# Kernel optimization log

Measured on AMD Instinct MI355X. Metric: run time of the kernel, lower is better.

## Reference

```python
import jax, jax.numpy as jnp
import numpy as np
from math import sqrt

D_MODEL = 1024
NUM_HEADS = 16
MASK_VAL = -100000000.0


def setup_inputs() -> dict:
    key = jax.random.key(0)
    k1, k2, k3, k4, k5 = jax.random.split(key, 5)
    scale = 1.0 / sqrt(D_MODEL)
    return {
        "in_features": jax.random.normal(k1, (2, 2048, D_MODEL), dtype=jnp.float32),
        "q_proj_weight": jax.random.normal(k2, (D_MODEL, D_MODEL), dtype=jnp.float32) * scale,
        "k_proj_weight": jax.random.normal(k3, (D_MODEL, D_MODEL), dtype=jnp.float32) * scale,
        "v_proj_weight": jax.random.normal(k4, (D_MODEL, D_MODEL), dtype=jnp.float32) * scale,
        "o_proj_weight": jax.random.normal(k5, (D_MODEL, D_MODEL), dtype=jnp.float32) * scale,
    }


def _proj_heads(x, w, h):
    # x: [b, s, d_in], w: [h*d, d_in] -> [b, h, s, d]
    d = w.shape[0] // h
    w = w.reshape(h, d, w.shape[1])
    return jnp.einsum('bsi,hdi->bhsd', x, w)


def reference(in_features, q_proj_weight, k_proj_weight, v_proj_weight, o_proj_weight):
    h = NUM_HEADS
    b, s, _ = in_features.shape
    q = _proj_heads(in_features, q_proj_weight, h)  # [b,h,s,dk]
    k = _proj_heads(in_features, k_proj_weight, h)
    v = _proj_heads(in_features, v_proj_weight, h)
    d_k = q.shape[-1]
    # additive causal mask: -1e8 above diagonal
    mask = jnp.triu(jnp.full((s, s), MASK_VAL, dtype=q.dtype), k=1)[None, None]
    scores = jnp.einsum('bhqd,bhkd->bhqk', q, k) / sqrt(d_k) + mask
    attn = jax.nn.softmax(scores, axis=-1)
    out = jnp.einsum('bhqk,bhkd->bhqd', attn, v)          # [b,h,s,dv]
    out = out.transpose(0, 2, 1, 3).reshape(b, s, -1)      # [b,s,h*dv]
    return jnp.einsum('bsv,mv->bsm', out, o_proj_weight)
```

## Files before the change

### kernel.cpp

```cpp
#include <hip/hip_runtime.h>
#include <hip/hip_bf16.h>
#include <stdint.h>
#include <type_traits>

typedef __bf16 bf16;
typedef __bf16 bf16x4 __attribute__((ext_vector_type(4)));
typedef __bf16 bf16x8 __attribute__((ext_vector_type(8)));
typedef float floatx4 __attribute__((ext_vector_type(4)));
typedef unsigned int u32;

#define D_MODEL 1024
#define SEQ 2048
#define NHEADS 16
#define DH 64
#define BATCH 2
#define MROWS (BATCH * SEQ)

#define XELEMS ((size_t)MROWS * D_MODEL)
#define WELEMS ((size_t)D_MODEL * D_MODEL)
#define CVT_ELEMS (XELEMS + 4 * WELEMS)

__device__ __forceinline__ void gload_lds16(const void* g, void* l) {
  __builtin_amdgcn_global_load_lds(
      (const __attribute__((address_space(1))) u32*)g,
      (__attribute__((address_space(3))) u32*)l, 16, 0, 0);
}

__global__ __launch_bounds__(256) void cvt_f32_bf16(
    const float* __restrict__ s0, const float* __restrict__ s1,
    const float* __restrict__ s2, const float* __restrict__ s3,
    const float* __restrict__ s4, bf16* __restrict__ dst) {
  const size_t i = ((size_t)blockIdx.x * 256 + threadIdx.x) * 8;
  const float* src;
  size_t off;
  if (i < XELEMS) {
    src = s0; off = i;
  } else {
    const size_t j = i - XELEMS;
    const int r = (int)(j / WELEMS);
    src = (r == 0) ? s1 : (r == 1) ? s2 : (r == 2) ? s3 : s4;
    off = j - (size_t)r * WELEMS;
  }
  floatx4 f0 = *(const floatx4*)&src[off];
  floatx4 f1 = *(const floatx4*)&src[off + 4];
  bf16x8 o;
#pragma unroll
  for (int j = 0; j < 4; j++) { o[j] = (bf16)f0[j]; o[4 + j] = (bf16)f1[j]; }
  *(bf16x8*)&dst[i] = o;
}


__global__ __launch_bounds__(256) void gemm_qkv(
    const bf16* __restrict__ A, const bf16* __restrict__ Wq,
    const bf16* __restrict__ Wk, const bf16* __restrict__ Wv,
    bf16* __restrict__ Qo, bf16* __restrict__ Ko, bf16* __restrict__ Vto) {
  const int z = blockIdx.z;
  const bf16* W = (z == 0) ? Wq : (z == 1) ? Wk : Wv;

  __shared__ bf16 As[128 * 64];
  __shared__ bf16 Bs[128 * 64];

  const int tid = threadIdx.x;
  const int lane = tid & 63;
  const int w = tid >> 6;
  const int lo16 = lane & 15;
  const int quad = lane >> 4;
  const int wy = w >> 1, wx = w & 1;

  const int m0 = blockIdx.y * 128;
  const int n0 = blockIdx.x * 128;

  const int sl = lane >> 3;
  const int sc = ((lane & 7) ^ sl) * 8;

  const floatx4 fz = {0.f, 0.f, 0.f, 0.f};
  floatx4 acc[4][4];
#pragma unroll
  for (int i = 0; i < 4; i++)
#pragma unroll
    for (int j = 0; j < 4; j++) acc[i][j] = fz;

  auto kloop = [&](auto vt) {
    constexpr bool VT = decltype(vt)::value;
    for (int k0 = 0; k0 < 1024; k0 += 64) {
      __syncthreads();
#pragma unroll
      for (int i = 0; i < 4; i++) {
        const int seg = i * 4 + w;
        const int row = seg * 8 + sl;
        gload_lds16(&A[(size_t)(m0 + row) * 1024 + k0 + sc], &As[seg * 512]);
        gload_lds16(&W[(size_t)(n0 + row) * 1024 + k0 + sc], &Bs[seg * 512]);
      }
      __syncthreads();

#pragma unroll
      for (int kk = 0; kk < 64; kk += 32) {
        bf16x8 af[4], bfr[4];
        const int cc = (kk >> 3) + quad;
#pragma unroll
        for (int t = 0; t < 4; t++) {
          const int ra = wy * 64 + t * 16 + lo16;
          const int rb = wx * 64 + t * 16 + lo16;
          af[t]  = *(const bf16x8*)&As[ra * 64 + ((cc ^ (ra & 7)) << 3)];
          bfr[t] = *(const bf16x8*)&Bs[rb * 64 + ((cc ^ (rb & 7)) << 3)];
        }
#pragma unroll
        for (int mt = 0; mt < 4; mt++)
#pragma unroll
          for (int nt = 0; nt < 4; nt++) {
            if constexpr (VT)
              acc[mt][nt] = __builtin_amdgcn_mfma_f32_16x16x32_bf16(bfr[nt], af[mt], acc[mt][nt], 0, 0, 0);
            else
              acc[mt][nt] = __builtin_amdgcn_mfma_f32_16x16x32_bf16(af[mt], bfr[nt], acc[mt][nt], 0, 0, 0);
          }
      }
    }
  };
  if (z == 2) kloop(std::true_type{}); else kloop(std::false_type{});

  if (z < 2) {
    bf16* C = (z == 0) ? Qo : Ko;
#pragma unroll
    for (int mt = 0; mt < 4; mt++)
#pragma unroll
      for (int nt = 0; nt < 4; nt++)
#pragma unroll
        for (int r = 0; r < 4; r++) {
          const int row = m0 + wy * 64 + mt * 16 + quad * 4 + r;
          const int col = n0 + wx * 64 + nt * 16 + lo16;
          C[(size_t)row * D_MODEL + col] = (bf16)acc[mt][nt][r];
        }
  } else {
#pragma unroll
    for (int mt = 0; mt < 4; mt++)
#pragma unroll
      for (int nt = 0; nt < 4; nt++)
#pragma unroll
        for (int r = 0; r < 4; r++) {
          const int feat = n0 + wx * 64 + nt * 16 + quad * 4 + r;
          const int tok  = m0 + wy * 64 + mt * 16 + lo16;
          const int hh = feat >> 6, dd = feat & 63;
          const int bb = tok >> 11, ss = tok & 2047;
          Vto[(size_t)((bb * NHEADS + hh) * DH + dd) * SEQ + ss] = (bf16)acc[mt][nt][r];
        }
  }
}

__global__ __launch_bounds__(256) void gemm_o(
    const bf16* __restrict__ A, const bf16* __restrict__ W,
    float* __restrict__ C) {
  __shared__ bf16 As[2 * 64 * 64];
  __shared__ bf16 Bs[2 * 128 * 64];

  const int tid = threadIdx.x;
  const int lane = tid & 63;
  const int w = tid >> 6;
  const int lo16 = lane & 15;
  const int quad = lane >> 4;
  const int wy = w >> 1, wx = w & 1;

  const int m0 = blockIdx.y * 64;
  const int n0 = blockIdx.x * 128;

  const int sl = lane >> 3;
  const int sc = ((lane & 7) ^ sl) * 8;

  const floatx4 fz = {0.f, 0.f, 0.f, 0.f};
  floatx4 acc[2][4];
#pragma unroll
  for (int i = 0; i < 2; i++)
#pragma unroll
    for (int j = 0; j < 4; j++) acc[i][j] = fz;

  for (int k0 = 0; k0 < 1024; k0 += 128) {
    __syncthreads();
#pragma unroll
    for (int kh = 0; kh < 2; kh++) {
#pragma unroll
      for (int i = 0; i < 2; i++) {
        const int seg = i * 4 + w;
        const int row = seg * 8 + sl;
        gload_lds16(&A[(size_t)(m0 + row) * 1024 + k0 + kh * 64 + sc],
                    &As[kh * 4096 + seg * 512]);
      }
#pragma unroll
      for (int i = 0; i < 4; i++) {
        const int seg = i * 4 + w;
        const int row = seg * 8 + sl;
        gload_lds16(&W[(size_t)(n0 + row) * 1024 + k0 + kh * 64 + sc],
                    &Bs[kh * 8192 + seg * 512]);
      }
    }
    __syncthreads();

#pragma unroll
    for (int kk = 0; kk < 128; kk += 32) {
      const int kh = kk >> 6;
      const int cc = ((kk & 63) >> 3) + quad;
      bf16x8 af[2], bfr[4];
#pragma unroll
      for (int t = 0; t < 2; t++) {
        const int ra = wy * 32 + t * 16 + lo16;
        af[t] = *(const bf16x8*)&As[kh * 4096 + ra * 64 + ((cc ^ (ra & 7)) << 3)];
      }
#pragma unroll
      for (int t = 0; t < 4; t++) {
        const int rb = wx * 64 + t * 16 + lo16;
        bfr[t] = *(const bf16x8*)&Bs[kh * 8192 + rb * 64 + ((cc ^ (rb & 7)) << 3)];
      }
#pragma unroll
      for (int mt = 0; mt < 2; mt++)
#pragma unroll
        for (int nt = 0; nt < 4; nt++)
          acc[mt][nt] = __builtin_amdgcn_mfma_f32_16x16x32_bf16(af[mt], bfr[nt], acc[mt][nt], 0, 0, 0);
    }
  }

#pragma unroll
  for (int mt = 0; mt < 2; mt++)
#pragma unroll
    for (int nt = 0; nt < 4; nt++)
#pragma unroll
      for (int r = 0; r < 4; r++) {
        const int row = m0 + wy * 32 + mt * 16 + quad * 4 + r;
        const int col = n0 + wx * 64 + nt * 16 + lo16;
        C[(size_t)row * D_MODEL + col] = acc[mt][nt][r];
      }
}

#define LP 72

__global__ __launch_bounds__(512) void attn_causal(
    const bf16* __restrict__ Q, const bf16* __restrict__ Kg,
    const bf16* __restrict__ Vt, bf16* __restrict__ O) {
  __shared__ bf16 Ks[64 * LP];
  __shared__ bf16 VTs[64 * LP];
  __shared__ bf16 Ps[8][16 * LP];
  __shared__ float Es[4][64][40];

  const int tid = threadIdx.x;
  const int lane = tid & 63;
  const int wid = tid >> 6;
  const int g = wid >> 2;
  const int w4 = wid & 3;
  const int lo16 = lane & 15;
  const int quad = lane >> 4;

  const int x = blockIdx.x;
  const int qtA = x;
  const int qtB = 31 - x;
  const int tmax = qtB;
  const int h = blockIdx.y;
  const int b = blockIdx.z;
  const size_t base  = (size_t)b * SEQ * D_MODEL + (size_t)h * DH;
  const size_t baset = (size_t)(b * NHEADS + h) * DH * SEQ;

  const int rA = qtA * 64 + w4 * 16 + lo16;
  const int rB = qtB * 64 + w4 * 16 + lo16;
  bf16x8 qfA[2], qfB[2];
#pragma unroll
  for (int ks = 0; ks < 2; ks++) {
    qfA[ks] = *(const bf16x8*)&Q[base + (size_t)rA * D_MODEL + ks * 32 + quad * 8];
    qfB[ks] = *(const bf16x8*)&Q[base + (size_t)rB * D_MODEL + ks * 32 + quad * 8];
  }

  bf16x8 onesf;
#pragma unroll
  for (int j = 0; j < 8; j++) onesf[j] = (bf16)1.0f;

  const floatx4 fz = {0.f, 0.f, 0.f, 0.f};
  floatx4 oA[4], oB[4];
  floatx4 lA = fz, lB = fz;
#pragma unroll
  for (int i = 0; i < 4; i++) { oA[i] = fz; oB[i] = fz; }

  const int kr = tid >> 3;
  const int kc = (tid & 7) * 8;

  bf16x8 kv, vv;
  kv = *(const bf16x8*)&Kg[base + (size_t)kr * D_MODEL + kc];
  vv = *(const bf16x8*)&Vt[baset + (size_t)kr * SEQ + kc];

  for (int t = 0; t <= tmax; t++) {
    const int j0 = t * 64;
    __syncthreads();
    *(bf16x8*)&Ks[kr * LP + kc] = kv;
    *(bf16x8*)&VTs[kr * LP + kc] = vv;
    __syncthreads();

    if (t < tmax) {
      const int j1 = j0 + 64;
      kv = *(const bf16x8*)&Kg[base + (size_t)(j1 + kr) * D_MODEL + kc];
      vv = *(const bf16x8*)&Vt[baset + (size_t)kr * SEQ + j1 + kc];
    }

    bf16x8 kf[2][2], vf[4];
#pragma unroll
    for (int n = 0; n < 2; n++)
#pragma unroll
      for (int ks = 0; ks < 2; ks++)
        kf[n][ks] = *(const bf16x8*)&Ks[((2 * g + n) * 16 + lo16) * LP + ks * 32 + quad * 8];
#pragma unroll
    for (int dt = 0; dt < 4; dt++)
      vf[dt] = *(const bf16x8*)&VTs[(dt * 16 + lo16) * LP + g * 32 + quad * 8];

    auto compute = [&](int q0s, const bf16x8* qf, floatx4* oacc, floatx4& lacc,
                       bool diag) {
      floatx4 sacc[2];
#pragma unroll
      for (int n = 0; n < 2; n++) sacc[n] = fz;
#pragma unroll
      for (int n = 0; n < 2; n++)
#pragma unroll
        for (int ks = 0; ks < 2; ks++)
          sacc[n] = __builtin_amdgcn_mfma_f32_16x16x32_bf16(kf[n][ks], qf[ks], sacc[n], 0, 0, 0);

      if (diag) {
        const int myq = q0s + w4 * 16 + lo16;
#pragma unroll
        for (int n = 0; n < 2; n++) {
          const int kvb = j0 + (2 * g + n) * 16 + quad * 4;
          bf16x4 pk;
#pragma unroll
          for (int r = 0; r < 4; r++) {
            const float e = __builtin_amdgcn_exp2f(fmaf(sacc[n][r], 0.18033688f, -17.3123405f));
            pk[r] = (bf16)((kvb + r > myq) ? 0.f : e);
          }
          *(bf16x4*)&Ps[wid][lo16 * LP + n * 16 + quad * 4] = pk;
        }
      } else {
#pragma unroll
        for (int n = 0; n < 2; n++) {
          bf16x4 pk;
#pragma unroll
          for (int r = 0; r < 4; r++)
            pk[r] = (bf16)__builtin_amdgcn_exp2f(fmaf(sacc[n][r], 0.18033688f, -17.3123405f));
          *(bf16x4*)&Ps[wid][lo16 * LP + n * 16 + quad * 4] = pk;
        }
      }

      bf16x8 pf = *(const bf16x8*)&Ps[wid][lo16 * LP + quad * 8];
#pragma unroll
      for (int dt = 0; dt < 4; dt++)
        oacc[dt] = __builtin_amdgcn_mfma_f32_16x16x32_bf16(pf, vf[dt], oacc[dt], 0, 0, 0);
      lacc = __builtin_amdgcn_mfma_f32_16x16x32_bf16(pf, onesf, lacc, 0, 0, 0);
    };

    compute(qtB * 64, qfB, oB, lB, t == qtB);
    if (t <= qtA) compute(qtA * 64, qfA, oA, lA, t == qtA);
  }

  if (g == 1) {
    float* e = Es[w4][lane];
#pragma unroll
    for (int dt = 0; dt < 4; dt++)
#pragma unroll
      for (int r = 0; r < 4; r++) e[dt * 4 + r] = oA[dt][r];
#pragma unroll
    for (int r = 0; r < 4; r++) e[16 + r] = lA[r];
#pragma unroll
    for (int dt = 0; dt < 4; dt++)
#pragma unroll
      for (int r = 0; r < 4; r++) e[20 + dt * 4 + r] = oB[dt][r];
#pragma unroll
    for (int r = 0; r < 4; r++) e[36 + r] = lB[r];
  }
  __syncthreads();
  if (g == 0) {
    const float* e = Es[w4][lane];
#pragma unroll
    for (int dt = 0; dt < 4; dt++)
#pragma unroll
      for (int r = 0; r < 4; r++) { oA[dt][r] += e[dt * 4 + r]; oB[dt][r] += e[20 + dt * 4 + r]; }
#pragma unroll
    for (int r = 0; r < 4; r++) { lA[r] += e[16 + r]; lB[r] += e[36 + r]; }

    auto finish = [&](int q0s, floatx4* oacc, floatx4 lacc) {
#pragma unroll
      for (int r = 0; r < 4; r++) {
        const float inv = 1.0f / lacc[r];
        const int row = q0s + w4 * 16 + quad * 4 + r;
#pragma unroll
        for (int dt = 0; dt < 4; dt++)
          O[base + (size_t)row * D_MODEL + dt * 16 + lo16] = (bf16)(oacc[dt][r] * inv);
      }
    };
    finish(qtA * 64, oA, lA);
    finish(qtB * 64, oB, lB);
  }
}

extern "C" void kernel_launch(void* const* d_in, const int* in_sizes, int n_in,
                              void* d_out, int out_size, void* d_ws, size_t ws_size,
                              hipStream_t stream) {
  const float* X  = (const float*)d_in[0];
  const float* Wq = (const float*)d_in[1];
  const float* Wk = (const float*)d_in[2];
  const float* Wv = (const float*)d_in[3];
  const float* Wo = (const float*)d_in[4];
  float* out = (float*)d_out;

  bf16* cvt = (bf16*)d_ws;
  bf16* Xb  = cvt;
  bf16* Wqb = cvt + XELEMS;
  bf16* Wkb = Wqb + WELEMS;
  bf16* Wvb = Wkb + WELEMS;
  bf16* Wob = Wvb + WELEMS;
  bf16* Qb  = cvt + CVT_ELEMS;
  bf16* Kb  = Qb + XELEMS;
  bf16* Vtb = Kb + XELEMS;
  bf16* Ob  = Vtb + XELEMS;

  dim3 blk(256);
  cvt_f32_bf16<<<dim3((u32)(CVT_ELEMS / (256 * 8))), blk, 0, stream>>>(
      X, Wq, Wk, Wv, Wo, cvt);
  gemm_qkv<<<dim3(8, 32, 3), blk, 0, stream>>>(Xb, Wqb, Wkb, Wvb, Qb, Kb, Vtb);
  attn_causal<<<dim3(16, NHEADS, BATCH), dim3(512), 0, stream>>>(Qb, Kb, Vtb, Ob);
  gemm_o<<<dim3(8, 64), blk, 0, stream>>>(Ob, Wob, out);
}
```

Before: 179.5 us.

## Process 128-key chunks per iteration in causal attention, alias LDS buffers

The attention loop now stages 128 keys per iteration instead of 64, with each of the two warp groups handling 64 keys. This halves the number of barrier-separated load/store rounds and doubles the MFMA work done per synchronisation. K fragments and V fragments are now read from LDS inside the compute lambda. The LDS arrays are packed into one buffer, with the epilogue reduction area aliasing the K/V region, and launch bounds request 4 blocks per CU. The cost is extra masked work on diagonal chunks when the query tile covers only half of a chunk, plus more register pressure from four score accumulators.

After: 179.0 us. No clear change (-0.3%).

```diff
diff --git a/kernel.cpp b/kernel.cpp
--- a/kernel.cpp
+++ b/kernel.cpp
@@ -49,7 +49,6 @@
   *(bf16x8*)&dst[i] = o;
 }
 
-
 __global__ __launch_bounds__(256) void gemm_qkv(
     const bf16* __restrict__ A, const bf16* __restrict__ Wq,
     const bf16* __restrict__ Wk, const bf16* __restrict__ Wv,
@@ -228,15 +227,18 @@
       }
 }
 
-#define LP 72
-
-__global__ __launch_bounds__(512) void attn_causal(
+#define LPK 72
+#define LPV 136
+#define LPP 72
+
+__global__ __launch_bounds__(512, 4) void attn_causal(
     const bf16* __restrict__ Q, const bf16* __restrict__ Kg,
     const bf16* __restrict__ Vt, bf16* __restrict__ O) {
-  __shared__ bf16 Ks[64 * LP];
-  __shared__ bf16 VTs[64 * LP];
-  __shared__ bf16 Ps[8][16 * LP];
-  __shared__ float Es[4][64][40];
+  __shared__ __align__(16) char smem[54272];
+  bf16* Ks  = (bf16*)smem;
+  bf16* VTs = (bf16*)(smem + 18432);
+  bf16* Ps  = (bf16*)(smem + 35840);
+  float* Es = (float*)smem;
 
   const int tid = threadIdx.x;
   const int lane = tid & 63;
@@ -249,7 +251,8 @@
   const int x = blockIdx.x;
   const int qtA = x;
   const int qtB = 31 - x;
-  const int tmax = qtB;
+  const int nA = (qtA + 2) >> 1;
+  const int nB = (qtB + 2) >> 1;
   const int h = blockIdx.y;
   const int b = blockIdx.z;
   const size_t base  = (size_t)b * SEQ * D_MODEL + (size_t)h * DH;
@@ -277,81 +280,90 @@
   const int kr = tid >> 3;
   const int kc = (tid & 7) * 8;
 
-  bf16x8 kv, vv;
-  kv = *(const bf16x8*)&Kg[base + (size_t)kr * D_MODEL + kc];
-  vv = *(const bf16x8*)&Vt[baset + (size_t)kr * SEQ + kc];
-
-  for (int t = 0; t <= tmax; t++) {
-    const int j0 = t * 64;
+  bf16x8 kvp[2], vvp[2];
+#pragma unroll
+  for (int c2 = 0; c2 < 2; c2++) {
+    kvp[c2] = *(const bf16x8*)&Kg[base + (size_t)(c2 * 64 + kr) * D_MODEL + kc];
+    vvp[c2] = *(const bf16x8*)&Vt[baset + (size_t)kr * SEQ + c2 * 64 + kc];
+  }
+
+  for (int c = 0; c < nB; c++) {
+    const int j0 = c * 128;
     __syncthreads();
-    *(bf16x8*)&Ks[kr * LP + kc] = kv;
-    *(bf16x8*)&VTs[kr * LP + kc] = vv;
+#pragma unroll
+    for (int c2 = 0; c2 < 2; c2++) {
+      *(bf16x8*)&Ks[(c2 * 64 + kr) * LPK + kc] = kvp[c2];
+      *(bf16x8*)&VTs[kr * LPV + c2 * 64 + kc] = vvp[c2];
+    }
     __syncthreads();
 
-    if (t < tmax) {
-      const int j1 = j0 + 64;
-      kv = *(const bf16x8*)&Kg[base + (size_t)(j1 + kr) * D_MODEL + kc];
-      vv = *(const bf16x8*)&Vt[baset + (size_t)kr * SEQ + j1 + kc];
+    if (c + 1 < nB) {
+      const int j1 = j0 + 128;
+#pragma unroll
+      for (int c2 = 0; c2 < 2; c2++) {
+        kvp[c2] = *(const bf16x8*)&Kg[base + (size_t)(j1 + c2 * 64 + kr) * D_MODEL + kc];
+        vvp[c2] = *(const bf16x8*)&Vt[baset + (size_t)kr * SEQ + j1 + c2 * 64 + kc];
+      }
     }
-
-    bf16x8 kf[2][2], vf[4];
-#pragma unroll
-    for (int n = 0; n < 2; n++)
-#pragma unroll
-      for (int ks = 0; ks < 2; ks++)
-        kf[n][ks] = *(const bf16x8*)&Ks[((2 * g + n) * 16 + lo16) * LP + ks * 32 + quad * 8];
-#pragma unroll
-    for (int dt = 0; dt < 4; dt++)
-      vf[dt] = *(const bf16x8*)&VTs[(dt * 16 + lo16) * LP + g * 32 + quad * 8];
 
     auto compute = [&](int q0s, const bf16x8* qf, floatx4* oacc, floatx4& lacc,
                        bool diag) {
-      floatx4 sacc[2];
-#pragma unroll
-      for (int n = 0; n < 2; n++) sacc[n] = fz;
-#pragma unroll
-      for (int n = 0; n < 2; n++)
-#pragma unroll
-        for (int ks = 0; ks < 2; ks++)
-          sacc[n] = __builtin_amdgcn_mfma_f32_16x16x32_bf16(kf[n][ks], qf[ks], sacc[n], 0, 0, 0);
+      floatx4 sacc[4];
+#pragma unroll
+      for (int n = 0; n < 4; n++) sacc[n] = fz;
+#pragma unroll
+      for (int n = 0; n < 4; n++) {
+        const int rk = g * 64 + n * 16 + lo16;
+#pragma unroll
+        for (int ks = 0; ks < 2; ks++) {
+          bf16x8 kf = *(const bf16x8*)&Ks[rk * LPK + ks * 32 + quad * 8];
+          sacc[n] = __builtin_amdgcn_mfma_f32_16x16x32_bf16(kf, qf[ks], sacc[n], 0, 0, 0);
+        }
+      }
 
       if (diag) {
         const int myq = q0s + w4 * 16 + lo16;
 #pragma unroll
-        for (int n = 0; n < 2; n++) {
-          const int kvb = j0 + (2 * g + n) * 16 + quad * 4;
+        for (int n = 0; n < 4; n++) {
+          const int kvb = j0 + g * 64 + n * 16 + quad * 4;
           bf16x4 pk;
 #pragma unroll
           for (int r = 0; r < 4; r++) {
             const float e = __builtin_amdgcn_exp2f(fmaf(sacc[n][r], 0.18033688f, -17.3123405f));
             pk[r] = (bf16)((kvb + r > myq) ? 0.f : e);
           }
-          *(bf16x4*)&Ps[wid][lo16 * LP + n * 16 + quad * 4] = pk;
+          *(bf16x4*)&Ps[wid * 1152 + lo16 * LPP + n * 16 + quad * 4] = pk;
         }
       } else {
 #pragma unroll
-        for (int n = 0; n < 2; n++) {
+        for (int n = 0; n < 4; n++) {
           bf16x4 pk;
 #pragma unroll
           for (int r = 0; r < 4; r++)
             pk[r] = (bf16)__builtin_amdgcn_exp2f(fmaf(sacc[n][r], 0.18033688f, -17.3123405f));
-          *(bf16x4*)&Ps[wid][lo16 * LP + n * 16 + quad * 4] = pk;
-        }
-      }
-
-      bf16x8 pf = *(const bf16x8*)&Ps[wid][lo16 * LP + quad * 8];
-#pragma unroll
-      for (int dt = 0; dt < 4; dt++)
-        oacc[dt] = __builtin_amdgcn_mfma_f32_16x16x32_bf16(pf, vf[dt], oacc[dt], 0, 0, 0);
-      lacc = __builtin_amdgcn_mfma_f32_16x16x32_bf16(pf, onesf, lacc, 0, 0, 0);
+          *(bf16x4*)&Ps[wid * 1152 + lo16 * LPP + n * 16 + quad * 4] = pk;
+        }
+      }
+
+#pragma unroll
+      for (int ks = 0; ks < 2; ks++) {
+        bf16x8 pf = *(const bf16x8*)&Ps[wid * 1152 + lo16 * LPP + ks * 32 + quad * 8];
+#pragma unroll
+        for (int dt = 0; dt < 4; dt++) {
+          bf16x8 vf = *(const bf16x8*)&VTs[(dt * 16 + lo16) * LPV + g * 64 + ks * 32 + quad * 8];
+          oacc[dt] = __builtin_amdgcn_mfma_f32_16x16x32_bf16(pf, vf, oacc[dt], 0, 0, 0);
+        }
+        lacc = __builtin_amdgcn_mfma_f32_16x16x32_bf16(pf, onesf, lacc, 0, 0, 0);
+      }
     };
 
-    compute(qtB * 64, qfB, oB, lB, t == qtB);
-    if (t <= qtA) compute(qtA * 64, qfA, oA, lA, t == qtA);
-  }
-
+    compute(qtB * 64, qfB, oB, lB, c == nB - 1);
+    if (c < nA) compute(qtA * 64, qfA, oA, lA, c == nA - 1);
+  }
+
+  __syncthreads();
   if (g == 1) {
-    float* e = Es[w4][lane];
+    float* e = &Es[(w4 * 64 + lane) * 40];
 #pragma unroll
     for (int dt = 0; dt < 4; dt++)
 #pragma unroll
@@ -367,7 +379,7 @@
   }
   __syncthreads();
   if (g == 0) {
-    const float* e = Es[w4][lane];
+    const float* e = &Es[(w4 * 64 + lane) * 40];
 #pragma unroll
     for (int dt = 0; dt < 4; dt++)
 #pragma unroll
```
